# Performance work log

Hardware: AMD Instinct MI355X
Metric: run time of the kernel (lower is better)

Reference implementation:

```python
import jax, jax.numpy as jnp
import numpy as np

D_MODEL = 1024
NHEAD = 16
H_DIM = D_MODEL // NHEAD  # 64


def setup_inputs() -> dict:
    key = jax.random.key(0)
    ks = jax.random.split(key, 11)
    B, S = 4, 2048
    s_in = 1.0 / np.sqrt(D_MODEL)
    return {
        "query": jax.random.normal(ks[0], (B, S, D_MODEL), jnp.float32),
        "key": jax.random.normal(ks[1], (B, S, D_MODEL), jnp.float32),
        "value": jax.random.normal(ks[2], (B, S, D_MODEL), jnp.float32),
        # per-head Q/K/V linear weights stacked over heads: [H, d_model, h_dim]
        "Wq": jax.random.normal(ks[3], (NHEAD, D_MODEL, H_DIM), jnp.float32) * s_in,
        "bq": jax.random.normal(ks[4], (NHEAD, H_DIM), jnp.float32) * 0.01,
        "Wk": jax.random.normal(ks[5], (NHEAD, D_MODEL, H_DIM), jnp.float32) * s_in,
        "bk": jax.random.normal(ks[6], (NHEAD, H_DIM), jnp.float32) * 0.01,
        "Wv": jax.random.normal(ks[7], (NHEAD, D_MODEL, H_DIM), jnp.float32) * s_in,
        "bv": jax.random.normal(ks[8], (NHEAD, H_DIM), jnp.float32) * 0.01,
        "Wp": jax.random.normal(ks[9], (D_MODEL, D_MODEL), jnp.float32) * s_in,
        "bp": jax.random.normal(ks[10], (D_MODEL,), jnp.float32) * 0.01,
    }


def reference(query, key, value, Wq, bq, Wk, bk, Wv, bv, Wp, bp):
    # Batched per-head projections (equivalent to the per-head Linear loop).
    q = jnp.einsum('bsd,hdk->bhsk', query, Wq) + bq[None, :, None, :]
    k = jnp.einsum('bsd,hdk->bhsk', key, Wk) + bk[None, :, None, :]
    v = jnp.einsum('bsd,hdk->bhsk', value, Wv) + bv[None, :, None, :]
    scale = 1.0 / jnp.sqrt(jnp.asarray(H_DIM, q.dtype))
    scores = jnp.einsum('bhik,bhjk->bhij', q, k) * scale  # [B,H,S,S]
    attn = jax.nn.softmax(scores, axis=-1)
    out = jnp.einsum('bhij,bhjk->bhik', attn, v)  # [B,H,S,h_dim]
    # Concatenate heads along the feature dim (head-major order = torch.cat dim=2).
    B, H, S, K = out.shape
    out = out.transpose(0, 2, 1, 3).reshape(B, S, H * K)
    return out @ Wp + bp
```

## Files before the change

### kernel.cpp

```cpp
#include <hip/hip_runtime.h>

namespace {
constexpr int DM = 1024;
constexpr int NH = 16;
constexpr int SEQ = 2048;
constexpr int NB = 4;
constexpr int ROWS = NB * SEQ;

typedef float f32x4 __attribute__((ext_vector_type(4)));
typedef short bf16x8 __attribute__((ext_vector_type(8)));

#define WAITCNT(s) asm volatile("s_waitcnt " s ::: "memory")
#define SCHED_BAR() __builtin_amdgcn_sched_barrier(0)

__device__ inline ushort f2bf(float x) {
  union { float f; unsigned u; } v; v.f = x;
  unsigned r = v.u + 0x7fffu + ((v.u >> 16) & 1u);
  return (ushort)(r >> 16);
}

__device__ inline unsigned cvt_pk_bf16(float lo, float hi) {
  unsigned r;
  asm("v_cvt_pk_bf16_f32 %0, %1, %2" : "=v"(r) : "v"(lo), "v"(hi));
  return r;
}

__device__ inline float fast_exp2(float x) {
  float r;
  asm("v_exp_f32 %0, %1" : "=v"(r) : "v"(x));
  return r;
}

__device__ inline float max3f(float a, float b, float c) {
  float r;
  asm("v_max3_f32 %0, %1, %2, %3" : "=v"(r) : "v"(a), "v"(b), "v"(c));
  return r;
}

__device__ inline bf16x8 pack8(float4 a, float4 b) {
  union { bf16x8 v; unsigned u[4]; } t;
  t.u[0] = cvt_pk_bf16(a.x, a.y); t.u[1] = cvt_pk_bf16(a.z, a.w);
  t.u[2] = cvt_pk_bf16(b.x, b.y); t.u[3] = cvt_pk_bf16(b.z, b.w);
  return t.v;
}

__device__ inline void glds16(const void* g, void* l) {
  __builtin_amdgcn_global_load_lds(
      (const __attribute__((address_space(1))) void*)g,
      (__attribute__((address_space(3))) void*)l, 16, 0, 0);
}

__global__ __launch_bounds__(256) void cvt3(
    const float* __restrict__ q, const float* __restrict__ k,
    const float* __restrict__ v, ushort* __restrict__ oq,
    ushort* __restrict__ ok, ushort* __restrict__ ov)
{
  const int z = blockIdx.y;
  const float* src = (z == 0) ? q : (z == 1) ? k : v;
  ushort* dst = (z == 0) ? oq : (z == 1) ? ok : ov;
  const int n8 = ROWS * DM / 8;
  for (int i = blockIdx.x * 256 + threadIdx.x; i < n8; i += gridDim.x * 256) {
    const float4 a = *reinterpret_cast<const float4*>(src + (size_t)i * 8);
    const float4 b = *reinterpret_cast<const float4*>(src + (size_t)i * 8 + 4);
    *reinterpret_cast<bf16x8*>(dst + (size_t)i * 8) = pack8(a, b);
  }
}

__global__ __launch_bounds__(256) void prep_w4(
    const float* __restrict__ Wq, const float* __restrict__ Wk,
    const float* __restrict__ Wv, const float* __restrict__ Wp,
    ushort* __restrict__ Wtq, ushort* __restrict__ Wtk,
    ushort* __restrict__ Wtv, ushort* __restrict__ Wtp)
{
  __shared__ ushort T[64][72];
  const int z = blockIdx.z;
  const float* W = (z == 0) ? Wq : (z == 1) ? Wk : (z == 2) ? Wv : Wp;
  ushort* Wt = (z == 0) ? Wtq : (z == 1) ? Wtk : (z == 2) ? Wtv : Wtp;
  const int mode = (z == 3) ? 1 : 0;
  const int t = threadIdx.x;
  const int d0 = blockIdx.x * 64;
  const int colbase = blockIdx.y * 64;
  #pragma unroll
  for (int pass = 0; pass < 4; ++pass) {
    const int dl = (t >> 4) + pass * 16;
    const int k = (t & 15) * 4;
    const size_t src = (mode == 0)
        ? (size_t)colbase * 1024 + (size_t)(d0 + dl) * 64 + k
        : (size_t)(d0 + dl) * 1024 + colbase + k;
    const float4 v = *reinterpret_cast<const float4*>(W + src);
    T[k + 0][dl] = f2bf(v.x); T[k + 1][dl] = f2bf(v.y);
    T[k + 2][dl] = f2bf(v.z); T[k + 3][dl] = f2bf(v.w);
  }
  __syncthreads();
  const int k = t >> 2, dp = (t & 3) * 16;
  ushort* dst = Wt + (size_t)(colbase + k) * DM + d0 + dp;
  #pragma unroll
  for (int j = 0; j < 16; ++j) dst[j] = T[k][dp + j];
}

__global__ __launch_bounds__(256) void repack_v(
    const ushort* __restrict__ Vn, ushort* __restrict__ Vp)
{
  __shared__ ushort T[64][80];
  const int kt = blockIdx.x, bh = blockIdx.y;
  const int tid = threadIdx.x;
  {
    const int kv = tid >> 2, hd0 = (tid & 3) * 16;
    const ushort* src = Vn + ((size_t)bh * SEQ + kt * 64 + kv) * 64 + hd0;
    *reinterpret_cast<bf16x8*>(&T[kv][hd0]) = *reinterpret_cast<const bf16x8*>(src);
    *reinterpret_cast<bf16x8*>(&T[kv][hd0 + 8]) =
        *reinterpret_cast<const bf16x8*>(src + 8);
  }
  __syncthreads();
  const int hd = tid >> 2, g = tid & 3;
  const int sw = (hd & 7) << 1;
  ushort buf[16];
  #pragma unroll
  for (int cc = 0; cc < 4; ++cc) {
    const int j = (g * 4 + cc) ^ sw;
    #pragma unroll
    for (int t = 0; t < 4; ++t) buf[cc * 4 + t] = T[j + 16 * t][hd];
  }
  ushort* dst = Vp + ((size_t)bh * 32 + kt) * 4096 + hd * 64 + g * 16;
  *reinterpret_cast<bf16x8*>(dst) = *reinterpret_cast<const bf16x8*>(&buf[0]);
  *reinterpret_cast<bf16x8*>(dst + 8) = *reinterpret_cast<const bf16x8*>(&buf[8]);
}

template<int OMODE>
__device__ __forceinline__ void gemm_body(
    const ushort* __restrict__ A, const ushort* __restrict__ Bt,
    const float* __restrict__ bias, void* __restrict__ Out, float oscale)
{
  __shared__ ushort As[128 * 64];
  __shared__ ushort Bs[128 * 64];
  const int tid = threadIdx.x;
  const int l = tid & 63, l15 = l & 15, l4 = l >> 4;
  const int wid = tid >> 6, wm = wid >> 1, wn = wid & 1;
  const int col0 = blockIdx.x * 128, row0 = blockIdx.y * 128;
  f32x4 acc[4][4] = {};

  const int gr = (wid << 5) + (l >> 3);
  const int gc = l & 7;
  const int gsw = (l >> 3) & 7;
  const ushort* bsrc[4];
  const ushort* asrc[4];
  int ldst[4];
  #pragma unroll
  for (int i = 0; i < 4; ++i) {
    bsrc[i] = Bt + (size_t)(col0 + gr + i * 8) * DM + ((gc ^ gsw) << 3);
    asrc[i] = A + (size_t)(row0 + gr + i * 8) * DM + ((gc ^ gsw) << 3);
    ldst[i] = (wid * 32 + i * 8) * 64;
  }

  for (int t = 0; t < 16; ++t) {
    const int k0 = t * 64;
    #pragma unroll
    for (int i = 0; i < 4; ++i) glds16(asrc[i] + k0, &As[ldst[i]]);
    #pragma unroll
    for (int i = 0; i < 4; ++i) glds16(bsrc[i] + k0, &Bs[ldst[i]]);
    __syncthreads();

    __builtin_amdgcn_s_setprio(1);
    #pragma unroll
    for (int kc = 0; kc < 2; ++kc) {
      bf16x8 a[4], bfr[4];
      #pragma unroll
      for (int m = 0; m < 4; ++m) {
        const int rr = wm * 64 + m * 16 + l15;
        a[m] = *reinterpret_cast<const bf16x8*>(
            &As[rr * 64 + (((kc * 4 + l4) ^ (rr & 7)) << 3)]);
      }
      #pragma unroll
      for (int n = 0; n < 4; ++n) {
        const int cc = wn * 64 + n * 16 + l15;
        bfr[n] = *reinterpret_cast<const bf16x8*>(
            &Bs[cc * 64 + (((kc * 4 + l4) ^ (cc & 7)) << 3)]);
      }
      #pragma unroll
      for (int m = 0; m < 4; ++m)
        #pragma unroll
        for (int n = 0; n < 4; ++n)
          acc[m][n] = __builtin_amdgcn_mfma_f32_16x16x32_bf16(
              a[m], bfr[n], acc[m][n], 0, 0, 0);
    }
    __builtin_amdgcn_s_setprio(0);
    __syncthreads();
  }

  #pragma unroll
  for (int m = 0; m < 4; ++m) {
    #pragma unroll
    for (int n = 0; n < 4; ++n) {
      const int col = col0 + wn * 64 + n * 16 + l15;
      const float bz = bias[col];
      #pragma unroll
      for (int r = 0; r < 4; ++r) {
        const int row = row0 + wm * 64 + m * 16 + l4 * 4 + r;
        const float v = (acc[m][n][r] + bz) * oscale;
        if (OMODE == 0) {
          const size_t o =
              ((size_t)((row >> 11) * NH + (col >> 6)) * SEQ + (row & 2047)) * 64
              + (col & 63);
          ((ushort*)Out)[o] = f2bf(v);
        } else {
          ((float*)Out)[(size_t)row * DM + col] = v;
        }
      }
    }
  }
}

__global__ __launch_bounds__(256) void gemm_qkv(
    const ushort* __restrict__ Aq, const ushort* __restrict__ Ak,
    const ushort* __restrict__ Av, const ushort* __restrict__ Bq,
    const ushort* __restrict__ Bk, const ushort* __restrict__ Bv,
    const float* __restrict__ bq, const float* __restrict__ bk,
    const float* __restrict__ bv, ushort* __restrict__ Oq,
    ushort* __restrict__ Ok, ushort* __restrict__ Ov)
{
  constexpr float SC = 0.125f * 1.44269504088896340736f;
  const int z = blockIdx.z;
  const ushort* A = (z == 0) ? Aq : (z == 1) ? Ak : Av;
  const ushort* B = (z == 0) ? Bq : (z == 1) ? Bk : Bv;
  const float* bi = (z == 0) ? bq : (z == 1) ? bk : bv;
  ushort* O = (z == 0) ? Oq : (z == 1) ? Ok : Ov;
  gemm_body<0>(A, B, bi, O, (z == 0) ? SC : 1.0f);
}

__global__ __launch_bounds__(256) void gemm_out(
    const ushort* __restrict__ A, const ushort* __restrict__ Bt,
    const float* __restrict__ bias, float* __restrict__ Out)
{
  gemm_body<3>(A, Bt, bias, Out, 1.0f);
}

__global__ __launch_bounds__(512) void attn_mfma(
    const ushort* __restrict__ Q, const ushort* __restrict__ K,
    const ushort* __restrict__ Vp, ushort* __restrict__ AO)
{
  __shared__ ushort Ks[2][64 * 64];
  __shared__ ushort Vs[2][64 * 64];
  __shared__ ushort Pl[8 * 16 * 64];
  const int tid = threadIdx.x;
  const int w = tid >> 6, l = tid & 63;
  const int l15 = l & 15, l4 = l >> 4;
  const int h = blockIdx.y, b = blockIdx.z;
  const int bh = b * NH + h;
  const int qbase = blockIdx.x * 128 + w * 16;
  ushort* Pw = Pl + w * (16 * 64);
  const int swzv = (l15 & 7) << 1;

  bf16x8 qf[2];
  {
    const ushort* qp = Q + ((size_t)bh * SEQ + qbase + l15) * 64 + l4 * 8;
    qf[0] = *reinterpret_cast<const bf16x8*>(qp);
    qf[1] = *reinterpret_cast<const bf16x8*>(qp + 32);
  }
  bf16x8 ones;
  {
    union { bf16x8 v; ushort u[8]; } t;
    #pragma unroll
    for (int i = 0; i < 8; ++i) t.u[i] = 0x3F80;
    ones = t.v;
  }

  const int krow = (w << 3) + (l >> 3);
  const int kch = l & 7;
  const ushort* ksrc = K + ((size_t)bh * SEQ + krow) * 64 + ((kch ^ (krow & 7)) << 3);
  const ushort* vsrc = Vp + (size_t)bh * (32 * 4096) + w * 512 + (l << 3);
  const int kvdst = w * 512;

  f32x4 oacc[4] = {};
  f32x4 lacc = {};
  float m2[4];
  #pragma unroll
  for (int r = 0; r < 4; ++r) m2[r] = -1e30f;

  glds16(ksrc, &Ks[0][kvdst]);
  glds16(vsrc, &Vs[0][kvdst]);
  glds16(ksrc + 4096, &Ks[1][kvdst]);
  glds16(vsrc + 4096, &Vs[1][kvdst]);

  for (int kt = 0; kt < 32; ++kt) {
    const int p = kt & 1;
    WAITCNT("vmcnt(2)");
    SCHED_BAR();
    __builtin_amdgcn_s_barrier();
    SCHED_BAR();

    f32x4 sacc[4] = {};
    __builtin_amdgcn_s_setprio(1);
    #pragma unroll
    for (int kc = 0; kc < 2; ++kc) {
      #pragma unroll
      for (int c = 0; c < 4; ++c) {
        const int kvi = c * 16 + l15;
        const bf16x8 bf = *reinterpret_cast<const bf16x8*>(
            &Ks[p][kvi * 64 + (((kc * 4 + l4) ^ (kvi & 7)) << 3)]);
        sacc[c] = __builtin_amdgcn_mfma_f32_16x16x32_bf16(qf[kc], bf, sacc[c], 0, 0, 0);
      }
    }
    __builtin_amdgcn_s_setprio(0);

    #pragma unroll
    for (int r = 0; r < 4; ++r) {
      const float s0 = sacc[0][r], s1 = sacc[1][r];
      const float s2 = sacc[2][r], s3 = sacc[3][r];
      const float pmax = fmaxf(max3f(s0, s1, s2), s3);
      if (!__all(pmax <= m2[r] + 8.f)) {
        float t = pmax;
        t = fmaxf(t, __shfl_xor(t, 1));
        t = fmaxf(t, __shfl_xor(t, 2));
        t = fmaxf(t, __shfl_xor(t, 4));
        t = fmaxf(t, __shfl_xor(t, 8));
        const float mn = fmaxf(m2[r], t);
        const float corr = fast_exp2(m2[r] - mn);
        m2[r] = mn;
        lacc[r] *= corr;
        #pragma unroll
        for (int c = 0; c < 4; ++c) oacc[c][r] *= corr;
      }
      const float p0 = fast_exp2(s0 - m2[r]);
      const float p1 = fast_exp2(s1 - m2[r]);
      const float p2 = fast_exp2(s2 - m2[r]);
      const float p3 = fast_exp2(s3 - m2[r]);
      const unsigned w0 = cvt_pk_bf16(p0, p1);
      const unsigned w1 = cvt_pk_bf16(p2, p3);
      const int q = l4 * 4 + r;
      *reinterpret_cast<uint2*>(
          &Pw[q * 64 + ((l15 ^ ((q & 7) << 1)) << 2)]) = make_uint2(w0, w1);
    }

    __builtin_amdgcn_s_setprio(1);
    #pragma unroll
    for (int kc = 0; kc < 2; ++kc) {
      const int cbk = 2 * (kc * 4 + l4);
      const bf16x8 af = *reinterpret_cast<const bf16x8*>(
          &Pw[l15 * 64 + ((cbk ^ swzv) << 2)]);
      lacc = __builtin_amdgcn_mfma_f32_16x16x32_bf16(af, ones, lacc, 0, 0, 0);
      #pragma unroll
      for (int c = 0; c < 4; ++c) {
        const int hd = c * 16 + l15;
        const bf16x8 bf = *reinterpret_cast<const bf16x8*>(
            &Vs[p][hd * 64 + ((cbk ^ swzv) << 2)]);
        oacc[c] = __builtin_amdgcn_mfma_f32_16x16x32_bf16(af, bf, oacc[c], 0, 0, 0);
      }
    }
    __builtin_amdgcn_s_setprio(0);

    __builtin_amdgcn_s_barrier();
    SCHED_BAR();
    const int ktn = (kt + 2 < 32) ? kt + 2 : 31;
    glds16(ksrc + (size_t)ktn * 4096, &Ks[p][kvdst]);
    glds16(vsrc + (size_t)ktn * 4096, &Vs[p][kvdst]);
  }

  #pragma unroll
  for (int r = 0; r < 4; ++r) {
    const float inv = 1.f / lacc[r];
    const int s = qbase + l4 * 4 + r;
    #pragma unroll
    for (int c = 0; c < 4; ++c) {
      AO[((size_t)b * SEQ + s) * DM + h * 64 + c * 16 + l15] =
          f2bf(oacc[c][r] * inv);
    }
  }
}

}

extern "C" void kernel_launch(void* const* d_in, const int* in_sizes, int n_in,
                              void* d_out, int out_size, void* d_ws, size_t ws_size,
                              hipStream_t stream) {
  const float* query = (const float*)d_in[0];
  const float* key   = (const float*)d_in[1];
  const float* value = (const float*)d_in[2];
  const float* Wq    = (const float*)d_in[3];
  const float* bq    = (const float*)d_in[4];
  const float* Wk    = (const float*)d_in[5];
  const float* bk    = (const float*)d_in[6];
  const float* Wv    = (const float*)d_in[7];
  const float* bv    = (const float*)d_in[8];
  const float* Wp    = (const float*)d_in[9];
  const float* bp    = (const float*)d_in[10];
  float* out = (float*)d_out;

  char* ws = (char*)d_ws;
  const size_t MB = 1024 * 1024;
  ushort* Wtq = (ushort*)(ws + 0 * MB);
  ushort* Wtk = (ushort*)(ws + 2 * MB);
  ushort* Wtv = (ushort*)(ws + 4 * MB);
  ushort* Wtp = (ushort*)(ws + 6 * MB);
  ushort* Qa  = (ushort*)(ws + 8 * MB);
  ushort* Ka  = (ushort*)(ws + 24 * MB);
  ushort* Va  = (ushort*)(ws + 40 * MB);
  ushort* Qb  = (ushort*)(ws + 56 * MB);
  ushort* Kb  = (ushort*)(ws + 72 * MB);
  ushort* Vn  = (ushort*)(ws + 88 * MB);
  ushort* Vp  = (ushort*)(ws + 8 * MB);
  ushort* AO  = (ushort*)(ws + 24 * MB);

  cvt3<<<dim3(1024, 3), 256, 0, stream>>>(query, key, value, Qa, Ka, Va);
  prep_w4<<<dim3(16, 16, 4), 256, 0, stream>>>(Wq, Wk, Wv, Wp, Wtq, Wtk, Wtv, Wtp);

  gemm_qkv<<<dim3(8, 64, 3), 256, 0, stream>>>(
      Qa, Ka, Va, Wtq, Wtk, Wtv, bq, bk, bv, Qb, Kb, Vn);

  repack_v<<<dim3(32, 64), 256, 0, stream>>>(Vn, Vp);

  attn_mfma<<<dim3(SEQ / 128, NH, NB), dim3(512), 0, stream>>>(Qb, Kb, Vp, AO);

  gemm_out<<<dim3(8, 64), 256, 0, stream>>>(AO, Wtp, bp, out);
}
```

Measured before the change: 236.0 us.

## Fuse V repack into QKV GEMM epilogue and add XCD-aware block remapping

Removes the separate repack_v kernel. The V-projection GEMM blocks now stage their bf16 output tile in shared memory and write it straight into the swizzled transposed layout that the attention kernel reads, which saves one launch and a full read and write of V. It also remaps block indices in both GEMMs and in the attention kernel so that neighbouring tiles land on the same XCD, aiming for better L2 reuse. The cost is a shared-memory round trip in the V epilogue, an extra barrier, and a strided LDS gather that may cause bank conflicts.

```diff
diff --git a/kernel.cpp b/kernel.cpp
--- a/kernel.cpp
+++ b/kernel.cpp
@@ -98,45 +98,17 @@
   for (int j = 0; j < 16; ++j) dst[j] = T[k][dp + j];
 }
 
-__global__ __launch_bounds__(256) void repack_v(
-    const ushort* __restrict__ Vn, ushort* __restrict__ Vp)
-{
-  __shared__ ushort T[64][80];
-  const int kt = blockIdx.x, bh = blockIdx.y;
-  const int tid = threadIdx.x;
-  {
-    const int kv = tid >> 2, hd0 = (tid & 3) * 16;
-    const ushort* src = Vn + ((size_t)bh * SEQ + kt * 64 + kv) * 64 + hd0;
-    *reinterpret_cast<bf16x8*>(&T[kv][hd0]) = *reinterpret_cast<const bf16x8*>(src);
-    *reinterpret_cast<bf16x8*>(&T[kv][hd0 + 8]) =
-        *reinterpret_cast<const bf16x8*>(src + 8);
-  }
-  __syncthreads();
-  const int hd = tid >> 2, g = tid & 3;
-  const int sw = (hd & 7) << 1;
-  ushort buf[16];
-  #pragma unroll
-  for (int cc = 0; cc < 4; ++cc) {
-    const int j = (g * 4 + cc) ^ sw;
-    #pragma unroll
-    for (int t = 0; t < 4; ++t) buf[cc * 4 + t] = T[j + 16 * t][hd];
-  }
-  ushort* dst = Vp + ((size_t)bh * 32 + kt) * 4096 + hd * 64 + g * 16;
-  *reinterpret_cast<bf16x8*>(dst) = *reinterpret_cast<const bf16x8*>(&buf[0]);
-  *reinterpret_cast<bf16x8*>(dst + 8) = *reinterpret_cast<const bf16x8*>(&buf[8]);
-}
-
 template<int OMODE>
 __device__ __forceinline__ void gemm_body(
-    const ushort* __restrict__ A, const ushort* __restrict__ Bt,
-    const float* __restrict__ bias, void* __restrict__ Out, float oscale)
-{
-  __shared__ ushort As[128 * 64];
-  __shared__ ushort Bs[128 * 64];
+    ushort* __restrict__ SMEM, const ushort* __restrict__ A,
+    const ushort* __restrict__ Bt, const float* __restrict__ bias,
+    void* __restrict__ Out, float oscale, int col0, int row0)
+{
+  ushort* As = SMEM;
+  ushort* Bs = SMEM + 8192;
   const int tid = threadIdx.x;
   const int l = tid & 63, l15 = l & 15, l4 = l >> 4;
   const int wid = tid >> 6, wm = wid >> 1, wn = wid & 1;
-  const int col0 = blockIdx.x * 128, row0 = blockIdx.y * 128;
   f32x4 acc[4][4] = {};
 
   const int gr = (wid << 5) + (l >> 3);
@@ -187,27 +159,68 @@
     __syncthreads();
   }
 
-  #pragma unroll
-  for (int m = 0; m < 4; ++m) {
-    #pragma unroll
-    for (int n = 0; n < 4; ++n) {
-      const int col = col0 + wn * 64 + n * 16 + l15;
-      const float bz = bias[col];
-      #pragma unroll
-      for (int r = 0; r < 4; ++r) {
-        const int row = row0 + wm * 64 + m * 16 + l4 * 4 + r;
-        const float v = (acc[m][n][r] + bz) * oscale;
-        if (OMODE == 0) {
-          const size_t o =
-              ((size_t)((row >> 11) * NH + (col >> 6)) * SEQ + (row & 2047)) * 64
-              + (col & 63);
-          ((ushort*)Out)[o] = f2bf(v);
-        } else {
-          ((float*)Out)[(size_t)row * DM + col] = v;
+  if (OMODE == 4) {
+    #pragma unroll
+    for (int m = 0; m < 4; ++m) {
+      #pragma unroll
+      for (int n = 0; n < 4; ++n) {
+        const int cl = wn * 64 + n * 16 + l15;
+        const float bz = bias[col0 + cl];
+        #pragma unroll
+        for (int r = 0; r < 4; ++r) {
+          const int sl = wm * 64 + m * 16 + l4 * 4 + r;
+          SMEM[sl * 128 + cl] = f2bf(acc[m][n][r] + bz);
         }
       }
     }
-  }
+    __syncthreads();
+    const int hd = tid & 63, ktl = (tid >> 6) & 1, hh = tid >> 7;
+    const int sw = (hd & 7) << 1;
+    const int bh = (row0 >> 11) * NH + (col0 >> 6) + hh;
+    const int ktg = ((row0 & 2047) >> 6) + ktl;
+    ushort* dst = (ushort*)Out + ((size_t)bh * 32 + ktg) * 4096 + hd * 64;
+    #pragma unroll
+    for (int ch = 0; ch < 8; ++ch) {
+      union { bf16x8 v; ushort u[8]; } pk;
+      #pragma unroll
+      for (int e = 0; e < 8; ++e) {
+        const int j = ch * 8 + e;
+        const int cp = j >> 2, tt = j & 3;
+        const int kv = (cp ^ sw) + 16 * tt;
+        pk.u[e] = SMEM[(ktl * 64 + kv) * 128 + hh * 64 + hd];
+      }
+      *reinterpret_cast<bf16x8*>(dst + ch * 8) = pk.v;
+    }
+  } else {
+    #pragma unroll
+    for (int m = 0; m < 4; ++m) {
+      #pragma unroll
+      for (int n = 0; n < 4; ++n) {
+        const int col = col0 + wn * 64 + n * 16 + l15;
+        const float bz = bias[col];
+        #pragma unroll
+        for (int r = 0; r < 4; ++r) {
+          const int row = row0 + wm * 64 + m * 16 + l4 * 4 + r;
+          const float v = (acc[m][n][r] + bz) * oscale;
+          if (OMODE == 0) {
+            const size_t o =
+                ((size_t)((row >> 11) * NH + (col >> 6)) * SEQ + (row & 2047)) * 64
+                + (col & 63);
+            ((ushort*)Out)[o] = f2bf(v);
+          } else {
+            ((float*)Out)[(size_t)row * DM + col] = v;
+          }
+        }
+      }
+    }
+  }
+}
+
+__device__ inline void xcd_remap_gemm(int& col0, int& row0) {
+  const int lin = blockIdx.x + (blockIdx.y << 3);
+  const int swz = (lin & 7) * 64 + (lin >> 3);
+  col0 = (swz & 7) * 128;
+  row0 = (swz >> 3) * 128;
 }
 
 __global__ __launch_bounds__(256) void gemm_qkv(
@@ -218,20 +231,24 @@
     const float* __restrict__ bv, ushort* __restrict__ Oq,
     ushort* __restrict__ Ok, ushort* __restrict__ Ov)
 {
+  __shared__ ushort SMEM[16384];
   constexpr float SC = 0.125f * 1.44269504088896340736f;
+  int col0, row0;
+  xcd_remap_gemm(col0, row0);
   const int z = blockIdx.z;
-  const ushort* A = (z == 0) ? Aq : (z == 1) ? Ak : Av;
-  const ushort* B = (z == 0) ? Bq : (z == 1) ? Bk : Bv;
-  const float* bi = (z == 0) ? bq : (z == 1) ? bk : bv;
-  ushort* O = (z == 0) ? Oq : (z == 1) ? Ok : Ov;
-  gemm_body<0>(A, B, bi, O, (z == 0) ? SC : 1.0f);
+  if (z == 0)      gemm_body<0>(SMEM, Aq, Bq, bq, Oq, SC,  col0, row0);
+  else if (z == 1) gemm_body<0>(SMEM, Ak, Bk, bk, Ok, 1.f, col0, row0);
+  else             gemm_body<4>(SMEM, Av, Bv, bv, Ov, 1.f, col0, row0);
 }
 
 __global__ __launch_bounds__(256) void gemm_out(
     const ushort* __restrict__ A, const ushort* __restrict__ Bt,
     const float* __restrict__ bias, float* __restrict__ Out)
 {
-  gemm_body<3>(A, Bt, bias, Out, 1.0f);
+  __shared__ ushort SMEM[16384];
+  int col0, row0;
+  xcd_remap_gemm(col0, row0);
+  gemm_body<3>(SMEM, A, Bt, bias, Out, 1.f, col0, row0);
 }
 
 __global__ __launch_bounds__(512) void attn_mfma(
@@ -244,9 +261,11 @@
   const int tid = threadIdx.x;
   const int w = tid >> 6, l = tid & 63;
   const int l15 = l & 15, l4 = l >> 4;
-  const int h = blockIdx.y, b = blockIdx.z;
+  const int lin = blockIdx.x + (blockIdx.y << 4) + (blockIdx.z << 8);
+  const int swz = (lin & 7) * 128 + (lin >> 3);
+  const int bx = swz & 15, h = (swz >> 4) & 15, b = swz >> 8;
   const int bh = b * NH + h;
-  const int qbase = blockIdx.x * 128 + w * 16;
+  const int qbase = bx * 128 + w * 16;
   ushort* Pw = Pl + w * (16 * 64);
   const int swzv = (l15 & 7) << 1;
 
@@ -396,17 +415,14 @@
   ushort* Va  = (ushort*)(ws + 40 * MB);
   ushort* Qb  = (ushort*)(ws + 56 * MB);
   ushort* Kb  = (ushort*)(ws + 72 * MB);
-  ushort* Vn  = (ushort*)(ws + 88 * MB);
-  ushort* Vp  = (ushort*)(ws + 8 * MB);
-  ushort* AO  = (ushort*)(ws + 24 * MB);
+  ushort* Vp  = (ushort*)(ws + 88 * MB);
+  ushort* AO  = (ushort*)(ws + 8 * MB);
 
   cvt3<<<dim3(1024, 3), 256, 0, stream>>>(query, key, value, Qa, Ka, Va);
   prep_w4<<<dim3(16, 16, 4), 256, 0, stream>>>(Wq, Wk, Wv, Wp, Wtq, Wtk, Wtv, Wtp);
 
   gemm_qkv<<<dim3(8, 64, 3), 256, 0, stream>>>(
-      Qa, Ka, Va, Wtq, Wtk, Wtv, bq, bk, bv, Qb, Kb, Vn);
-
-  repack_v<<<dim3(32, 64), 256, 0, stream>>>(Vn, Vp);
+      Qa, Ka, Va, Wtq, Wtk, Wtv, bq, bk, bv, Qb, Kb, Vp);
 
   attn_mfma<<<dim3(SEQ / 128, NH, NB), dim3(512), 0, stream>>>(Qb, Kb, Vp, AO);
 
```

Result: faster. 215.5 us (-8.7%).
